# Performance work log

Hardware: AMD Instinct MI355X
Metric: run time of the kernel (lower is better)

Reference implementation:

```python
import jax, jax.numpy as jnp
import numpy as np

B, T = 64, 1024
V, E, H = 50000, 256, 256


def setup_inputs() -> dict:
    key = jax.random.key(0)
    ks = jax.random.split(key, 16)
    s = 0.05
    d = {
        "tokens": jax.random.randint(ks[0], (B, T), 0, V, dtype=jnp.int32),
        "embed": jax.random.normal(ks[1], (V, E), dtype=jnp.float32) * s,
    }
    dims = [E, E, 2 * H, 2 * H]
    names = ["fw1", "bw1", "fw2", "bw2"]
    for n, (name, din) in enumerate(zip(names, dims)):
        d[name + "_Wi"] = jax.random.normal(ks[2 + 3 * n], (din, 4 * H), dtype=jnp.float32) * s
        d[name + "_Wh"] = jax.random.normal(ks[3 + 3 * n], (H, 4 * H), dtype=jnp.float32) * s
        d[name + "_b"] = jnp.zeros((4 * H,), dtype=jnp.float32)
    d["Wd"] = jax.random.normal(ks[14], (2 * H, 1), dtype=jnp.float32) * s
    d["bd"] = jnp.zeros((1,), dtype=jnp.float32)
    return d


def _lstm(x, Wi, Wh, b):
    # x: [B, T, D] -> outputs h over time: [B, T, H]
    xW = jnp.einsum('btd,dk->btk', x, Wi) + b  # precompute input projections
    Bc, Hc = x.shape[0], Wh.shape[0]
    c0 = jnp.zeros((Bc, Hc), x.dtype)
    h0 = jnp.zeros((Bc, Hc), x.dtype)

    def step(carry, z_t):
        c, h = carry
        z = z_t + h @ Wh  # [B, 4H], gate order i,f,g,o (flax LSTMCell)
        i, f, g, o = jnp.split(z, 4, axis=-1)
        c = jax.nn.sigmoid(f) * c + jax.nn.sigmoid(i) * jnp.tanh(g)
        h = jax.nn.sigmoid(o) * jnp.tanh(c)
        return (c, h), h

    _, ys = jax.lax.scan(step, (c0, h0), xW.swapaxes(0, 1))  # scan over time
    return ys.swapaxes(0, 1)


def _bilstm(x, fWi, fWh, fb, bWi, bWh, bb):
    fwd = _lstm(x, fWi, fWh, fb)
    # all lengths == seq_len, so flip_sequences reduces to full time flip
    bwd = jnp.flip(_lstm(jnp.flip(x, 1), bWi, bWh, bb), 1)
    return jnp.concatenate([fwd, bwd], axis=-1)


def reference(tokens, embed,
              fw1_Wi, fw1_Wh, fw1_b, bw1_Wi, bw1_Wh, bw1_b,
              fw2_Wi, fw2_Wh, fw2_b, bw2_Wi, bw2_Wh, bw2_b,
              Wd, bd):
    x = embed[tokens]                                   # [B, T, E]
    x = _bilstm(x, fw1_Wi, fw1_Wh, fw1_b, bw1_Wi, bw1_Wh, bw1_b)  # [B, T, 2H]
    x = _bilstm(x, fw2_Wi, fw2_Wh, fw2_b, bw2_Wi, bw2_Wh, bw2_b)  # [B, T, 2H]
    logits = x[:, -1, :] @ Wd + bd                      # [B, 1]
    return jax.nn.sigmoid(logits).squeeze(-1)           # [B]
```

## Files before the change

### kernel.cpp

```cpp
#include <hip/hip_runtime.h>
#include <hip/hip_bf16.h>
#include <cstdint>
#include <cstddef>

typedef __attribute__((ext_vector_type(8))) short bf16x8;
typedef __attribute__((ext_vector_type(4))) short bf16x4;
typedef __attribute__((ext_vector_type(4))) float f32x4;
typedef __attribute__((ext_vector_type(4))) int   i32x4;
typedef __attribute__((ext_vector_type(8))) int   i32x8;
typedef unsigned long long u64;

#define LOG2E 1.442695041f

__device__ __forceinline__ float bf2f(short s){
  unsigned int u = ((unsigned int)(unsigned short)s) << 16;
  return __builtin_bit_cast(float, u);
}
__device__ __forceinline__ short f2bf(float f){
  return __builtin_bit_cast(short, __float2bfloat16(f));
}
__device__ __forceinline__ float sigm(float x){
  return __builtin_amdgcn_rcpf(1.f + __builtin_amdgcn_exp2f(-LOG2E * x));
}
__device__ __forceinline__ float tanh_(float x){
  return 1.f - 2.f * __builtin_amdgcn_rcpf(1.f + __builtin_amdgcn_exp2f(2.f * LOG2E * x));
}
__device__ __forceinline__ void wg_barrier(){
  asm volatile("s_waitcnt lgkmcnt(0)" ::: "memory");
  __builtin_amdgcn_s_barrier();
  asm volatile("" ::: "memory");
}
__device__ __forceinline__ int orig_col8(int np){
  int w = np >> 7, rem = np & 127, gate = rem >> 5, ul = rem & 31;
  return gate * 256 + w * 32 + ul;
}
__device__ __forceinline__ char f2fp8(float x){
  int pk = __builtin_amdgcn_cvt_pk_fp8_f32(x, x, 0, false);
  return (char)(pk & 0xff);
}

__global__ void k_prep_wipT(const float* __restrict__ Wi, short* __restrict__ outT, int K){
  int idx = blockIdx.x * 256 + threadIdx.x;
  int kv = K >> 3;
  int np = idx / kv, k0 = (idx % kv) * 8;
  int oc = orig_col8(np);
  bf16x8 v;
  #pragma unroll
  for (int j = 0; j < 8; ++j) v[j] = f2bf(Wi[(size_t)(k0 + j) * 1024 + oc]);
  *(bf16x8*)(outT + (size_t)np * K + k0) = v;
}

__global__ void k_prep_bias(const float* __restrict__ b, float* __restrict__ bp){
  int np = blockIdx.x * 256 + threadIdx.x;
  bp[np] = b[orig_col8(np)];
}

__global__ void k_prep_wht8(const float* __restrict__ Wh, u64* __restrict__ w8){
  int idx = blockIdx.x * 256 + threadIdx.x;
  int l = idx & 63, fk = idx >> 6;
  int kki = fk & 1, wn = fk >> 1;
  int oc = orig_col8(wn * 16 + (l & 15));
  int kbase = kki * 128 + ((l >> 4) << 5);
  u64* dst = w8 + (size_t)idx * 4;
  #pragma unroll
  for (int qq = 0; qq < 4; ++qq){
    u64 x = 0;
    #pragma unroll
    for (int j = 0; j < 8; ++j){
      unsigned int b = (unsigned char)f2fp8(Wh[(size_t)(kbase + qq * 8 + j) * 1024 + oc]);
      x |= ((u64)b) << (8 * j);
    }
    dst[qq] = x;
  }
}

__global__ void k_gather(const int* __restrict__ tokens, const float* __restrict__ embed,
                         short* __restrict__ x1t){
  int v = blockIdx.x * 256 + threadIdx.x;
  const int total = 64 * 1024 * 256 / 4;
  for (; v < total; v += gridDim.x * 256){
    int e = v * 4;
    int row = e >> 8, k = e & 255;
    int t = row >> 6, b = row & 63;
    int tok = tokens[b * 1024 + t];
    f32x4 f = *(const f32x4*)(embed + (size_t)tok * 256 + k);
    bf16x4 o4;
    #pragma unroll
    for (int j = 0; j < 4; ++j) o4[j] = f2bf(f[j]);
    *(bf16x4*)(x1t + e) = o4;
  }
}

template<int K>
__global__ __launch_bounds__(256)
void k_gemm(const short* __restrict__ A, const short* __restrict__ BT,
            const float* __restrict__ bias, float* __restrict__ xw){
  __shared__ short ldsA[128 * 72];
  __shared__ short ldsB[128 * 72];
  int tid = threadIdx.x;
  int l = tid & 63, wid = tid >> 6, wm = wid >> 1, wn = wid & 1;
  int M0 = blockIdx.x * 128, N0 = blockIdx.y * 128;
  f32x4 acc[4][4] = {};
  for (int kt = 0; kt < K / 64; ++kt){
    __syncthreads();
    for (int i = tid; i < 1024; i += 256){
      int row = i >> 3, seg = i & 7;
      *(bf16x8*)&ldsA[row * 72 + seg * 8] = *(const bf16x8*)&A[(size_t)(M0 + row) * K + kt * 64 + seg * 8];
      *(bf16x8*)&ldsB[row * 72 + seg * 8] = *(const bf16x8*)&BT[(size_t)(N0 + row) * K + kt * 64 + seg * 8];
    }
    __syncthreads();
    #pragma unroll
    for (int kk = 0; kk < 2; ++kk){
      int koff = kk * 32 + ((l >> 4) << 3);
      bf16x8 af[4], bfm[4];
      #pragma unroll
      for (int mt = 0; mt < 4; ++mt) af[mt] = *(const bf16x8*)&ldsA[(wm * 64 + mt * 16 + (l & 15)) * 72 + koff];
      #pragma unroll
      for (int nt = 0; nt < 4; ++nt) bfm[nt] = *(const bf16x8*)&ldsB[(wn * 64 + nt * 16 + (l & 15)) * 72 + koff];
      #pragma unroll
      for (int mt = 0; mt < 4; ++mt)
        #pragma unroll
        for (int nt = 0; nt < 4; ++nt)
          acc[mt][nt] = __builtin_amdgcn_mfma_f32_16x16x32_bf16(af[mt], bfm[nt], acc[mt][nt], 0, 0, 0);
    }
  }
  int t = blockIdx.x * 2 + wm;
  #pragma unroll
  for (int mt = 0; mt < 4; ++mt){
    #pragma unroll
    for (int nt = 0; nt < 4; ++nt){
      int ng = (N0 >> 4) + wn * 4 + nt;
      float bs = bias[ng * 16 + (l & 15)];
      f32x4 ov;
      #pragma unroll
      for (int r = 0; r < 4; ++r) ov[r] = acc[mt][nt][r] + bs;
      *(f32x4*)&xw[((size_t)(t * 4 + mt) * 64 + ng) * 256 + l * 4] = ov;
    }
  }
}

template<int WRITE_SEQ>
__global__ __launch_bounds__(512, 2)
void k_recur8(const float* __restrict__ xw_f, const float* __restrict__ xw_b,
              const u64* __restrict__ w8_f, const u64* __restrict__ w8_b,
              short* __restrict__ outp, float* __restrict__ cstate, char* __restrict__ hstate,
              int t0, int S, int two_dirs, int first)
{
  __shared__ char ldsH[12288];
  int g = blockIdx.x;
  int d  = two_dirs ? (g >> 2) : 0;
  int cb = two_dirs ? (g & 3) : g;
  int blk = g;
  const float* xw = d ? xw_b : xw_f;
  const u64*  w8  = d ? w8_b : w8_f;
  int tid = threadIdx.x, w = tid >> 6, l = tid & 63;

  i32x8 Breg[16];
  #pragma unroll
  for (int n = 0; n < 8; ++n)
    #pragma unroll
    for (int kki = 0; kki < 2; ++kki){
      const i32x4* bp = (const i32x4*)(w8 + ((size_t)((w * 8 + n) * 2 + kki) * 64 + l) * 4);
      Breg[n * 2 + kki] = __builtin_shufflevector(bp[0], bp[1], 0,1,2,3,4,5,6,7);
    }

  f32x4 cst[2];
  if (first){
    if (tid < 384) *(i32x4*)(ldsH + tid * 16) = i32x4{0,0,0,0};
    cst[0] = f32x4{0.f,0.f,0.f,0.f};
    cst[1] = f32x4{0.f,0.f,0.f,0.f};
  } else {
    const char* hsrc = hstate + (size_t)blk * 6144;
    if (tid < 384) *(i32x4*)(ldsH + tid * 16) = *(const i32x4*)(hsrc + tid * 16);
    #pragma unroll
    for (int uh = 0; uh < 2; ++uh)
      #pragma unroll
      for (int r = 0; r < 4; ++r){
        int batch = ((l >> 4) << 2) + r, unit = w * 32 + uh * 16 + (l & 15);
        cst[uh][r] = cstate[((size_t)blk * 16 + batch) * 256 + unit];
      }
  }
  __syncthreads();

  long xwStep = (d ? -1l : 1l) * 4 * 64 * 256;
  const float* xwCur = xw + ((size_t)((d ? (S - 1) : 0) * 4 + cb) * 64) * 256;
  f32x4 px[8];
  #pragma unroll
  for (int n = 0; n < 8; ++n)
    px[n] = *(const f32x4*)&xwCur[((w * 8 + n) * 64 + l) * 4];

  char* seqB = nullptr;
  long seqStepB = (d ? -1l : 1l) * 64 * 512 * 2;
  if (WRITE_SEQ)
    seqB = (char*)(outp + ((long)(d ? (1023 - t0) : t0) * 64 + cb * 16 + ((l >> 4) << 2)) * 512
                        + d * 256 + w * 32 + (l & 15));

  const int aOff = (l & 15) * 48 + ((l >> 4) * 768);
  const int hOff = w * 768 + ((l >> 4) << 2) * 48 + (l & 15);

  int p = 0;
  #pragma unroll 1
  for (int s = 0; s < S; ++s){
    const float* xwNext = (s + 1 < S) ? (xwCur + xwStep) : xwCur;

    const char* aB = ldsH + p * 6144 + aOff;
    i32x4 a0 = *(const i32x4*)(aB);
    i32x4 a1 = *(const i32x4*)(aB + 16);
    i32x4 a2 = *(const i32x4*)(aB + 3072);
    i32x4 a3 = *(const i32x4*)(aB + 3088);
    i32x8 af0 = __builtin_shufflevector(a0, a1, 0,1,2,3,4,5,6,7);
    i32x8 af1 = __builtin_shufflevector(a2, a3, 0,1,2,3,4,5,6,7);

    f32x4 acc[8];
    acc[0] = px[0]; acc[2] = px[2]; acc[4] = px[4]; acc[6] = px[6];
    #pragma unroll
    for (int n = 0; n < 8; n += 2){
      acc[n] = __builtin_amdgcn_mfma_scale_f32_16x16x128_f8f6f4(
                 af0, Breg[n * 2 + 0], acc[n], 0, 0, 0, 0x7f7f7f7f, 0, 0x7f7f7f7f);
      acc[n] = __builtin_amdgcn_mfma_scale_f32_16x16x128_f8f6f4(
                 af1, Breg[n * 2 + 1], acc[n], 0, 0, 0, 0x7f7f7f7f, 0, 0x7f7f7f7f);
    }
    acc[1] = px[1]; acc[3] = px[3]; acc[5] = px[5]; acc[7] = px[7];
    #pragma unroll
    for (int n = 0; n < 8; ++n)
      px[n] = *(const f32x4*)&xwNext[((w * 8 + n) * 64 + l) * 4];
    #pragma unroll
    for (int n = 1; n < 8; n += 2){
      acc[n] = __builtin_amdgcn_mfma_scale_f32_16x16x128_f8f6f4(
                 af0, Breg[n * 2 + 0], acc[n], 0, 0, 0, 0x7f7f7f7f, 0, 0x7f7f7f7f);
      acc[n] = __builtin_amdgcn_mfma_scale_f32_16x16x128_f8f6f4(
                 af1, Breg[n * 2 + 1], acc[n], 0, 0, 0, 0x7f7f7f7f, 0, 0x7f7f7f7f);
    }

    char* hw = ldsH + (p ^ 1) * 6144 + hOff;
    #pragma unroll
    for (int uh = 0; uh < 2; ++uh){
      #pragma unroll
      for (int r = 0; r < 4; ++r){
        float ii = sigm(acc[0 + uh][r]);
        float ff = sigm(acc[2 + uh][r]);
        float gg = tanh_(acc[4 + uh][r]);
        float oo = sigm(acc[6 + uh][r]);
        float cc = ff * cst[uh][r] + ii * gg;
        cst[uh][r] = cc;
        float hh = oo * tanh_(cc);
        *(char*)(hw + r * 48 + uh * 16) = f2fp8(hh);
        if (WRITE_SEQ){
          *(short*)(seqB + uh * 32 + r * 1024) = f2bf(hh);
        } else if (s == S - 1){
          outp[((size_t)cb * 16 + ((l >> 4) << 2) + r) * 256 + w * 32 + uh * 16 + (l & 15)] = f2bf(hh);
        }
      }
    }
    wg_barrier();
    p ^= 1;
    if (WRITE_SEQ) seqB += seqStepB;
    xwCur = xwNext;
  }

  {
    char* hdst = hstate + (size_t)blk * 6144;
    if (tid < 384) *(i32x4*)(hdst + tid * 16) = *(const i32x4*)(ldsH + p * 6144 + tid * 16);
  }
  #pragma unroll
  for (int uh = 0; uh < 2; ++uh)
    #pragma unroll
    for (int r = 0; r < 4; ++r){
      int batch = ((l >> 4) << 2) + r, unit = w * 32 + uh * 16 + (l & 15);
      cstate[((size_t)blk * 16 + batch) * 256 + unit] = cst[uh][r];
    }
}

__global__ void k_h2b(const short* __restrict__ x2t, const float* __restrict__ Wi,
                      const float* __restrict__ bias, float* __restrict__ h2b){
  __shared__ float xr[512];
  int b = blockIdx.x, tid = threadIdx.x;
  for (int i = tid; i < 512; i += 256) xr[i] = bf2f(x2t[((size_t)1023 * 64 + b) * 512 + i]);
  __syncthreads();
  int u = tid;
  float s0 = bias[u], s2 = bias[512 + u], s3 = bias[768 + u];
  for (int k = 0; k < 512; ++k){
    float x = xr[k];
    const float* wr = Wi + (size_t)k * 1024;
    s0 += x * wr[u];
    s2 += x * wr[512 + u]; s3 += x * wr[768 + u];
  }
  float cc = sigm(s0) * tanh_(s2);
  float hh = sigm(s3) * tanh_(cc);
  h2b[(size_t)b * 256 + u] = hh;
}

__global__ void k_logits(const short* __restrict__ h2f, const float* __restrict__ h2b,
                         const float* __restrict__ Wd, const float* __restrict__ bd,
                         float* __restrict__ out){
  int b = threadIdx.x;
  float s = bd[0];
  for (int k = 0; k < 256; ++k) s += bf2f(h2f[b * 256 + k]) * Wd[k];
  for (int k = 0; k < 256; ++k) s += h2b[(size_t)b * 256 + k] * Wd[256 + k];
  out[b] = sigm(s);
}

extern "C" void kernel_launch(void* const* d_in, const int* in_sizes, int n_in,
                              void* d_out, int out_size, void* d_ws, size_t ws_size,
                              hipStream_t stream)
{
  (void)in_sizes; (void)n_in; (void)out_size;
  const int*   tokens = (const int*)d_in[0];
  const float* embed  = (const float*)d_in[1];
  const float* fw1_Wi = (const float*)d_in[2];
  const float* fw1_Wh = (const float*)d_in[3];
  const float* fw1_b  = (const float*)d_in[4];
  const float* bw1_Wi = (const float*)d_in[5];
  const float* bw1_Wh = (const float*)d_in[6];
  const float* bw1_b  = (const float*)d_in[7];
  const float* fw2_Wi = (const float*)d_in[8];
  const float* fw2_Wh = (const float*)d_in[9];
  const float* fw2_b  = (const float*)d_in[10];
  const float* bw2_Wi = (const float*)d_in[11];
  const float* bw2_Wh = (const float*)d_in[12];
  const float* bw2_b  = (const float*)d_in[13];
  const float* Wd     = (const float*)d_in[14];
  const float* bd     = (const float*)d_in[15];
  float* out = (float*)d_out;

  auto total_for = [](int S)->size_t{
    size_t fixed = 33554432ull + 67108864ull
                 + 524288ull*2 + 1048576ull
                 + 262144ull*3
                 + 12288ull
                 + 131072ull + 49152ull
                 + 65536ull + 24576ull
                 + 32768ull + 65536ull + 65536ull;
    return fixed + 2ull * (size_t)S * 262144ull;
  };
  int S = 256;
  while (S > 32 && total_for(S) > ws_size) S >>= 1;
  int NC = 1024 / S;

  char* ws = (char*)d_ws;
  size_t o = 0;
  auto alloc = [&](size_t sz){ size_t r = o; o += (sz + 255) & ~(size_t)255; return r; };
  short* x1t    = (short*)(ws + alloc(64ull * 1024 * 256 * 2));
  short* x2t    = (short*)(ws + alloc(64ull * 1024 * 512 * 2));
  float* xwf    = (float*)(ws + alloc((size_t)S * 262144ull));
  float* xwb    = (float*)(ws + alloc((size_t)S * 262144ull));
  short* wipT1f = (short*)(ws + alloc(256ull * 1024 * 2));
  short* wipT1b = (short*)(ws + alloc(256ull * 1024 * 2));
  short* wipT2f = (short*)(ws + alloc(512ull * 1024 * 2));
  u64*   w81f   = (u64*)(ws + alloc(262144ull));
  u64*   w81b   = (u64*)(ws + alloc(262144ull));
  u64*   w82f   = (u64*)(ws + alloc(262144ull));
  float* bp1f   = (float*)(ws + alloc(1024 * 4));
  float* bp1b   = (float*)(ws + alloc(1024 * 4));
  float* bp2f   = (float*)(ws + alloc(1024 * 4));
  float* cst1   = (float*)(ws + alloc(2ull * 64 * 256 * 4));
  char*  hst1   = (char*)(ws + alloc(8ull * 6144));
  float* cst2   = (float*)(ws + alloc(64ull * 256 * 4));
  char*  hst2   = (char*)(ws + alloc(4ull * 6144));
  short* hst2bf = (short*)(ws + alloc(64ull * 256 * 2));
  float* h2b    = (float*)(ws + alloc(64ull * 256 * 4));

  k_prep_wipT<<<128, 256, 0, stream>>>(fw1_Wi, wipT1f, 256);
  k_prep_wipT<<<128, 256, 0, stream>>>(bw1_Wi, wipT1b, 256);
  k_prep_wipT<<<256, 256, 0, stream>>>(fw2_Wi, wipT2f, 512);
  k_prep_bias<<<4, 256, 0, stream>>>(fw1_b, bp1f);
  k_prep_bias<<<4, 256, 0, stream>>>(bw1_b, bp1b);
  k_prep_bias<<<4, 256, 0, stream>>>(fw2_b, bp2f);
  k_prep_wht8<<<32, 256, 0, stream>>>(fw1_Wh, w81f);
  k_prep_wht8<<<32, 256, 0, stream>>>(bw1_Wh, w81b);
  k_prep_wht8<<<32, 256, 0, stream>>>(fw2_Wh, w82f);

  k_gather<<<4096, 256, 0, stream>>>(tokens, embed, x1t);

  dim3 ggrid(S / 2, 8);

  for (int c = 0; c < NC; ++c){
    int t0 = c * S;
    const short* Af = x1t + (size_t)t0 * 64 * 256;
    const short* Ab = x1t + (size_t)(1024 - (c + 1) * S) * 64 * 256;
    k_gemm<256><<<ggrid, 256, 0, stream>>>(Af, wipT1f, bp1f, xwf);
    k_gemm<256><<<ggrid, 256, 0, stream>>>(Ab, wipT1b, bp1b, xwb);
    k_recur8<1><<<8, 512, 0, stream>>>(xwf, xwb, w81f, w81b,
                                       x2t, cst1, hst1, t0, S, 1, c == 0);
  }

  for (int c = 0; c < NC; ++c){
    int t0 = c * S;
    const short* A2 = x2t + (size_t)t0 * 64 * 512;
    k_gemm<512><<<ggrid, 256, 0, stream>>>(A2, wipT2f, bp2f, xwf);
    k_recur8<0><<<4, 512, 0, stream>>>(xwf, xwf, w82f, w82f,
                                       hst2bf, cst2, hst2, t0, S, 0, c == 0);
  }

  k_h2b<<<64, 256, 0, stream>>>(x2t, bw2_Wi, bw2_b, h2b);

  k_logits<<<1, 64, 0, stream>>>(hst2bf, h2b, Wd, bd, out);
}
```

Before: 4.284 ms.

## Overlap next-chunk input GEMM with LSTM recurrence in one fused launch

```diff
diff --git a/kernel.cpp b/kernel.cpp
--- a/kernel.cpp
+++ b/kernel.cpp
@@ -19,12 +19,14 @@
 __device__ __forceinline__ short f2bf(float f){
   return __builtin_bit_cast(short, __float2bfloat16(f));
 }
-__device__ __forceinline__ float sigm(float x){
-  return __builtin_amdgcn_rcpf(1.f + __builtin_amdgcn_exp2f(-LOG2E * x));
-}
-__device__ __forceinline__ float tanh_(float x){
-  return 1.f - 2.f * __builtin_amdgcn_rcpf(1.f + __builtin_amdgcn_exp2f(2.f * LOG2E * x));
-}
+__device__ __forceinline__ float sig_pre(float zp){
+  return __builtin_amdgcn_rcpf(1.f + __builtin_amdgcn_exp2f(zp));
+}
+__device__ __forceinline__ float tanh_pre(float zpp){
+  return 1.f - 2.f * __builtin_amdgcn_rcpf(1.f + __builtin_amdgcn_exp2f(zpp));
+}
+__device__ __forceinline__ float sigm(float x){ return sig_pre(-LOG2E * x); }
+__device__ __forceinline__ float tanh_(float x){ return tanh_pre(2.f * LOG2E * x); }
 __device__ __forceinline__ void wg_barrier(){
   asm volatile("s_waitcnt lgkmcnt(0)" ::: "memory");
   __builtin_amdgcn_s_barrier();
@@ -33,6 +35,10 @@
 __device__ __forceinline__ int orig_col8(int np){
   int w = np >> 7, rem = np & 127, gate = rem >> 5, ul = rem & 31;
   return gate * 256 + w * 32 + ul;
+}
+__device__ __forceinline__ float gate_scale(int np){
+  int gate = (np >> 5) & 3;
+  return (gate == 2) ? (2.f * LOG2E) : (-LOG2E);
 }
 __device__ __forceinline__ char f2fp8(float x){
   int pk = __builtin_amdgcn_cvt_pk_fp8_f32(x, x, 0, false);
@@ -44,22 +50,25 @@
   int kv = K >> 3;
   int np = idx / kv, k0 = (idx % kv) * 8;
   int oc = orig_col8(np);
+  float sc = gate_scale(np);
   bf16x8 v;
   #pragma unroll
-  for (int j = 0; j < 8; ++j) v[j] = f2bf(Wi[(size_t)(k0 + j) * 1024 + oc]);
+  for (int j = 0; j < 8; ++j) v[j] = f2bf(Wi[(size_t)(k0 + j) * 1024 + oc] * sc);
   *(bf16x8*)(outT + (size_t)np * K + k0) = v;
 }
 
 __global__ void k_prep_bias(const float* __restrict__ b, float* __restrict__ bp){
   int np = blockIdx.x * 256 + threadIdx.x;
-  bp[np] = b[orig_col8(np)];
+  bp[np] = b[orig_col8(np)] * gate_scale(np);
 }
 
 __global__ void k_prep_wht8(const float* __restrict__ Wh, u64* __restrict__ w8){
   int idx = blockIdx.x * 256 + threadIdx.x;
   int l = idx & 63, fk = idx >> 6;
   int kki = fk & 1, wn = fk >> 1;
-  int oc = orig_col8(wn * 16 + (l & 15));
+  int pc = wn * 16 + (l & 15);
+  int oc = orig_col8(pc);
+  float sc = gate_scale(pc);
   int kbase = kki * 128 + ((l >> 4) << 5);
   u64* dst = w8 + (size_t)idx * 4;
   #pragma unroll
@@ -67,7 +76,7 @@
     u64 x = 0;
     #pragma unroll
     for (int j = 0; j < 8; ++j){
-      unsigned int b = (unsigned char)f2fp8(Wh[(size_t)(kbase + qq * 8 + j) * 1024 + oc]);
+      unsigned int b = (unsigned char)f2fp8(Wh[(size_t)(kbase + qq * 8 + j) * 1024 + oc] * sc);
       x |= ((u64)b) << (8 * j);
     }
     dst[qq] = x;
@@ -92,14 +101,11 @@
 }
 
 template<int K>
-__global__ __launch_bounds__(256)
-void k_gemm(const short* __restrict__ A, const short* __restrict__ BT,
-            const float* __restrict__ bias, float* __restrict__ xw){
-  __shared__ short ldsA[128 * 72];
-  __shared__ short ldsB[128 * 72];
-  int tid = threadIdx.x;
+__device__ __forceinline__ void gemm_tile(const short* __restrict__ A, const short* __restrict__ BT,
+                                          const float* __restrict__ bias, float* __restrict__ xw,
+                                          int bx, int by, short* ldsA, short* ldsB, int tid){
   int l = tid & 63, wid = tid >> 6, wm = wid >> 1, wn = wid & 1;
-  int M0 = blockIdx.x * 128, N0 = blockIdx.y * 128;
+  int M0 = bx * 128, N0 = by * 128;
   f32x4 acc[4][4] = {};
   for (int kt = 0; kt < K / 64; ++kt){
     __syncthreads();
@@ -124,7 +130,7 @@
           acc[mt][nt] = __builtin_amdgcn_mfma_f32_16x16x32_bf16(af[mt], bfm[nt], acc[mt][nt], 0, 0, 0);
     }
   }
-  int t = blockIdx.x * 2 + wm;
+  int t = bx * 2 + wm;
   #pragma unroll
   for (int mt = 0; mt < 4; ++mt){
     #pragma unroll
@@ -139,14 +145,44 @@
   }
 }
 
-template<int WRITE_SEQ>
+template<int K>
+__global__ __launch_bounds__(256)
+void k_gemm(const short* __restrict__ A, const short* __restrict__ BT,
+            const float* __restrict__ bias, float* __restrict__ xw){
+  __shared__ short ldsA[128 * 72];
+  __shared__ short ldsB[128 * 72];
+  gemm_tile<K>(A, BT, bias, xw, blockIdx.x, blockIdx.y, ldsA, ldsB, threadIdx.x);
+}
+
+#define MFMA_SC(a, b, c) __builtin_amdgcn_mfma_scale_f32_16x16x128_f8f6f4( \
+    (a), (b), (c), 0, 0, 0, 0x7f7f7f7f, 0, 0x7f7f7f7f)
+
+template<int WRITE_SEQ, int GK>
 __global__ __launch_bounds__(512, 2)
-void k_recur8(const float* __restrict__ xw_f, const float* __restrict__ xw_b,
-              const u64* __restrict__ w8_f, const u64* __restrict__ w8_b,
-              short* __restrict__ outp, float* __restrict__ cstate, char* __restrict__ hstate,
-              int t0, int S, int two_dirs, int first)
+void k_fused(const float* __restrict__ xw_f, const float* __restrict__ xw_b,
+             const u64* __restrict__ w8_f, const u64* __restrict__ w8_b,
+             short* __restrict__ outp, float* __restrict__ cstate, char* __restrict__ hstate,
+             int t0, int S, int two_dirs, int first, int R,
+             const short* __restrict__ gA0, const short* __restrict__ gA1,
+             const short* __restrict__ gBT0, const short* __restrict__ gBT1,
+             const float* __restrict__ gb0, const float* __restrict__ gb1,
+             float* __restrict__ gxw0, float* __restrict__ gxw1)
 {
-  __shared__ char ldsH[12288];
+  extern __shared__ char smem[];
+  if ((int)blockIdx.x >= R){
+    int sub = threadIdx.x >> 8;
+    int tid = threadIdx.x & 255;
+    int tile = ((int)blockIdx.x - R) * 2 + sub;
+    int tpj = 4 * S;
+    int job = tile / tpj, tt = tile % tpj;
+    short* ldsA = (short*)(smem + sub * 36864);
+    short* ldsB = ldsA + 128 * 72;
+    gemm_tile<GK>(job ? gA1 : gA0, job ? gBT1 : gBT0, job ? gb1 : gb0,
+                  job ? gxw1 : gxw0, tt >> 3, tt & 7, ldsA, ldsB, tid);
+    return;
+  }
+
+  char* ldsH = smem;
   int g = blockIdx.x;
   int d  = two_dirs ? (g >> 2) : 0;
   int cb = two_dirs ? (g & 3) : g;
@@ -212,35 +248,30 @@
     i32x8 af1 = __builtin_shufflevector(a2, a3, 0,1,2,3,4,5,6,7);
 
     f32x4 acc[8];
-    acc[0] = px[0]; acc[2] = px[2]; acc[4] = px[4]; acc[6] = px[6];
-    #pragma unroll
-    for (int n = 0; n < 8; n += 2){
-      acc[n] = __builtin_amdgcn_mfma_scale_f32_16x16x128_f8f6f4(
-                 af0, Breg[n * 2 + 0], acc[n], 0, 0, 0, 0x7f7f7f7f, 0, 0x7f7f7f7f);
-      acc[n] = __builtin_amdgcn_mfma_scale_f32_16x16x128_f8f6f4(
-                 af1, Breg[n * 2 + 1], acc[n], 0, 0, 0, 0x7f7f7f7f, 0, 0x7f7f7f7f);
-    }
-    acc[1] = px[1]; acc[3] = px[3]; acc[5] = px[5]; acc[7] = px[7];
-    #pragma unroll
-    for (int n = 0; n < 8; ++n)
+    #pragma unroll
+    for (int n = 0; n < 8; n += 2)
+      acc[n] = MFMA_SC(af1, Breg[n * 2 + 1], MFMA_SC(af0, Breg[n * 2 + 0], px[n]));
+    #pragma unroll
+    for (int n = 0; n < 8; n += 2)
       px[n] = *(const f32x4*)&xwNext[((w * 8 + n) * 64 + l) * 4];
     #pragma unroll
-    for (int n = 1; n < 8; n += 2){
-      acc[n] = __builtin_amdgcn_mfma_scale_f32_16x16x128_f8f6f4(
-                 af0, Breg[n * 2 + 0], acc[n], 0, 0, 0, 0x7f7f7f7f, 0, 0x7f7f7f7f);
-      acc[n] = __builtin_amdgcn_mfma_scale_f32_16x16x128_f8f6f4(
-                 af1, Breg[n * 2 + 1], acc[n], 0, 0, 0, 0x7f7f7f7f, 0, 0x7f7f7f7f);
-    }
+    for (int n = 1; n < 8; n += 2)
+      acc[n] = MFMA_SC(af1, Breg[n * 2 + 1], MFMA_SC(af0, Breg[n * 2 + 0], px[n]));
 
     char* hw = ldsH + (p ^ 1) * 6144 + hOff;
     #pragma unroll
     for (int uh = 0; uh < 2; ++uh){
+      if (uh == 1){
+        #pragma unroll
+        for (int n = 1; n < 8; n += 2)
+          px[n] = *(const f32x4*)&xwNext[((w * 8 + n) * 64 + l) * 4];
+      }
       #pragma unroll
       for (int r = 0; r < 4; ++r){
-        float ii = sigm(acc[0 + uh][r]);
-        float ff = sigm(acc[2 + uh][r]);
-        float gg = tanh_(acc[4 + uh][r]);
-        float oo = sigm(acc[6 + uh][r]);
+        float ii = sig_pre(acc[0 + uh][r]);
+        float ff = sig_pre(acc[2 + uh][r]);
+        float gg = tanh_pre(acc[4 + uh][r]);
+        float oo = sig_pre(acc[6 + uh][r]);
         float cc = ff * cst[uh][r] + ii * gg;
         cst[uh][r] = cc;
         float hh = oo * tanh_(cc);
@@ -331,7 +362,7 @@
                  + 131072ull + 49152ull
                  + 65536ull + 24576ull
                  + 32768ull + 65536ull + 65536ull;
-    return fixed + 2ull * (size_t)S * 262144ull;
+    return fixed + 4ull * (size_t)S * 262144ull;
   };
   int S = 256;
   while (S > 32 && total_for(S) > ws_size) S >>= 1;
@@ -342,8 +373,11 @@
   auto alloc = [&](size_t sz){ size_t r = o; o += (sz + 255) & ~(size_t)255; return r; };
   short* x1t    = (short*)(ws + alloc(64ull * 1024 * 256 * 2));
   short* x2t    = (short*)(ws + alloc(64ull * 1024 * 512 * 2));
-  float* xwf    = (float*)(ws + alloc((size_t)S * 262144ull));
-  float* xwb    = (float*)(ws + alloc((size_t)S * 262144ull));
+  float* xf[2], *xb[2];
+  xf[0] = (float*)(ws + alloc((size_t)S * 262144ull));
+  xf[1] = (float*)(ws + alloc((size_t)S * 262144ull));
+  xb[0] = (float*)(ws + alloc((size_t)S * 262144ull));
+  xb[1] = (float*)(ws + alloc((size_t)S * 262144ull));
   short* wipT1f = (short*)(ws + alloc(256ull * 1024 * 2));
   short* wipT1b = (short*)(ws + alloc(256ull * 1024 * 2));
   short* wipT2f = (short*)(ws + alloc(512ull * 1024 * 2));
@@ -360,6 +394,10 @@
   short* hst2bf = (short*)(ws + alloc(64ull * 256 * 2));
   float* h2b    = (float*)(ws + alloc(64ull * 256 * 4));
 
+  const int LDS_FUSED = 73728;
+  hipFuncSetAttribute((const void*)&k_fused<1,256>, hipFuncAttributeMaxDynamicSharedMemorySize, LDS_FUSED);
+  hipFuncSetAttribute((const void*)&k_fused<0,512>, hipFuncAttributeMaxDynamicSharedMemorySize, LDS_FUSED);
+
   k_prep_wipT<<<128, 256, 0, stream>>>(fw1_Wi, wipT1f, 256);
   k_prep_wipT<<<128, 256, 0, stream>>>(bw1_Wi, wipT1b, 256);
   k_prep_wipT<<<256, 256, 0, stream>>>(fw2_Wi, wipT2f, 512);
@@ -374,22 +412,30 @@
 
   dim3 ggrid(S / 2, 8);
 
+  k_gemm<256><<<ggrid, 256, 0, stream>>>(x1t, wipT1f, bp1f, xf[0]);
+  k_gemm<256><<<ggrid, 256, 0, stream>>>(x1t + (size_t)(1024 - S) * 64 * 256, wipT1b, bp1b, xb[0]);
+
   for (int c = 0; c < NC; ++c){
-    int t0 = c * S;
-    const short* Af = x1t + (size_t)t0 * 64 * 256;
-    const short* Ab = x1t + (size_t)(1024 - (c + 1) * S) * 64 * 256;
-    k_gemm<256><<<ggrid, 256, 0, stream>>>(Af, wipT1f, bp1f, xwf);
-    k_gemm<256><<<ggrid, 256, 0, stream>>>(Ab, wipT1b, bp1b, xwb);
-    k_recur8<1><<<8, 512, 0, stream>>>(xwf, xwb, w81f, w81b,
-                                       x2t, cst1, hst1, t0, S, 1, c == 0);
-  }
-
+    int cur = c & 1, nxt = cur ^ 1;
+    int njobs = (c + 1 < NC) ? 2 : 0;
+    int G = njobs * 2 * S;
+    const short* gA0 = x1t + (size_t)(c + 1) * S * 64 * 256;
+    const short* gA1 = x1t + (size_t)(1024 - (size_t)(c + 2) * S) * 64 * 256;
+    if (njobs == 0){ gA0 = x1t; gA1 = x1t; }
+    k_fused<1,256><<<8 + G, 512, LDS_FUSED, stream>>>(
+        xf[cur], xb[cur], w81f, w81b, x2t, cst1, hst1, c * S, S, 1, c == 0, 8,
+        gA0, gA1, wipT1f, wipT1b, bp1f, bp1b, xf[nxt], xb[nxt]);
+  }
+
+  k_gemm<512><<<ggrid, 256, 0, stream>>>(x2t, wipT2f, bp2f, xf[0]);
   for (int c = 0; c < NC; ++c){
-    int t0 = c * S;
-    const short* A2 = x2t + (size_t)t0 * 64 * 512;
-    k_gemm<512><<<ggrid, 256, 0, stream>>>(A2, wipT2f, bp2f, xwf);
-    k_recur8<0><<<4, 512, 0, stream>>>(xwf, xwf, w82f, w82f,
-                                       hst2bf, cst2, hst2, t0, S, 0, c == 0);
+    int cur = c & 1, nxt = cur ^ 1;
+    int njobs = (c + 1 < NC) ? 1 : 0;
+    int G = njobs * 2 * S;
+    const short* gA0 = (njobs ? (const short*)(x2t + (size_t)(c + 1) * S * 64 * 512) : (const short*)x2t);
+    k_fused<0,512><<<4 + G, 512, LDS_FUSED, stream>>>(
+        xf[cur], xf[cur], w82f, w82f, hst2bf, cst2, hst2, c * S, S, 0, c == 0, 4,
+        gA0, gA0, wipT2f, wipT2f, bp2f, bp2f, xf[nxt], xf[nxt]);
   }
 
   k_h2b<<<64, 256, 0, stream>>>(x2t, bw2_Wi, bw2_b, h2b);
```

Result: faster. 3.609 ms (-15.7%).
